# Kernel optimization log

Hardware: AMD Instinct MI355X
Metric: run time of the kernel (lower is better)

Reference implementation:

```python
import jax, jax.numpy as jnp
import numpy as np

T, S, F, A = 256, 256, 1024, 256


def setup_inputs() -> dict:
    key = jax.random.key(0)
    ks = jax.random.split(key, 7)
    scale = 0.02
    return {
        "batch_data": jax.random.normal(ks[0], (T * S, F), dtype=jnp.float32),
        "a_w": jax.random.normal(ks[1], (F, A), dtype=jnp.float32) * scale,
        "a_b": jax.random.normal(ks[2], (A,), dtype=jnp.float32) * scale,
        "b_w": jax.random.normal(ks[3], (F, A), dtype=jnp.float32) * scale,
        "b_b": jax.random.normal(ks[4], (A,), dtype=jnp.float32) * scale,
        "g_w": jax.random.normal(ks[5], (F, F), dtype=jnp.float32) * scale,
        "g_b": jax.random.normal(ks[6], (F,), dtype=jnp.float32) * scale,
        "s": S,
        "t": T,
    }


def reference(batch_data, a_w, a_b, b_w, b_b, g_w, g_b, s, t):
    # Linear projections then reshape to (t, s, dim)
    theta = (batch_data @ a_w + a_b).reshape(t, s, -1)   # (t, s, A)
    phi = (batch_data @ b_w + b_b).reshape(t, s, -1)     # (t, s, A)
    feats = (batch_data @ g_w + g_b).reshape(t, s, -1)   # (t, s, F)
    # Per-t bilinear attention: theta @ phi^T, no softmax
    attn = jnp.einsum("tsa,tra->tsr", theta, phi)        # (t, s, s)
    results = jnp.einsum("tsr,trf->tsf", attn, feats)    # (t, s, F)
    return results / (s + t)
```

## Files before the change

### kernel.cpp

```cpp
#include <hip/hip_runtime.h>
#include <stdint.h>

#define TT 256
#define SS 256
#define FF 1024
#define AA 256

typedef __attribute__((ext_vector_type(8))) short short8;
typedef __attribute__((ext_vector_type(4))) float floatx4;

__device__ __forceinline__ unsigned short f2bf(float f) {
  unsigned int u = __float_as_uint(f);
  u += 0x7FFFu + ((u >> 16) & 1u);
  return (unsigned short)(u >> 16);
}

__device__ __forceinline__ void gl_lds16(const unsigned short* g, unsigned short* l) {
  __builtin_amdgcn_global_load_lds(
      (__attribute__((address_space(1))) void*)(g),
      (__attribute__((address_space(3))) void*)(l), 16, 0, 0);
}

__global__ void k_transpose_cvt(const float* __restrict__ W,
                                unsigned short* __restrict__ WT,
                                int K, int N) {
  __shared__ float tile[32][33];
  const int bk = blockIdx.x * 32, bn = blockIdx.y * 32;
  const int tx = threadIdx.x, ty = threadIdx.y;
  for (int i = ty; i < 32; i += 8)
    tile[i][tx] = W[(size_t)(bk + i) * N + bn + tx];
  __syncthreads();
  for (int i = ty; i < 32; i += 8)
    WT[(size_t)(bn + i) * K + bk + tx] = f2bf(tile[tx][i]);
}

__global__ __launch_bounds__(256) void k_cvt(const float* __restrict__ in,
                                             unsigned short* __restrict__ out,
                                             unsigned int n8) {
  unsigned int i = blockIdx.x * 256u + threadIdx.x;
  const unsigned int stride = gridDim.x * 256u;
  for (; i < n8; i += stride) {
    const size_t base = (size_t)i * 8;
    const floatx4 v0 = *(const floatx4*)(in + base);
    const floatx4 v1 = *(const floatx4*)(in + base + 4);
    ushort4 h0, h1;
    h0.x = f2bf(v0.x); h0.y = f2bf(v0.y); h0.z = f2bf(v0.z); h0.w = f2bf(v0.w);
    h1.x = f2bf(v1.x); h1.y = f2bf(v1.y); h1.z = f2bf(v1.z); h1.w = f2bf(v1.w);
    *(ushort4*)(out + base) = h0;
    *(ushort4*)(out + base + 4) = h1;
  }
}

__device__ __forceinline__ void stage_half(const unsigned short* G, int ld,
                                           unsigned short* L, int tid) {
  const int wave = tid >> 6, lane = tid & 63;
#pragma unroll
  for (int c = 0; c < 2; ++c) {
    const int chunk = c * 8 + wave;
    const int r = chunk * 8 + (lane >> 3);
    const int k8 = (lane & 7) ^ (lane >> 3);
    gl_lds16(G + (size_t)r * ld + k8 * 8, L + chunk * 512);
  }
}

__device__ __forceinline__ short8 ldsfrag(const unsigned short* h, int row,
                                          int col) {
  return *(const short8*)&h[row * 64 + (col ^ ((row & 7) << 3))];
}

#define KLOOP_256(Ap, ldA, Bp, ldB, NKT)                                       \
  for (int kt = 0; kt < (NKT); ++kt) {                                         \
    const unsigned short* Ah = As + ((kt & 1) * 2 + wm) * 8192;                \
    const unsigned short* Bh = Bs + ((kt & 1) * 2 + (wn >> 1)) * 8192;         \
    const int nbuf = 1 - (kt & 1);                                             \
    if (kt + 1 < (NKT)) {                                                      \
      stage_half((Ap) + (size_t)(kt + 1) * 64, (ldA),                          \
                 As + (nbuf * 2 + 0) * 8192, tid);                             \
      asm volatile("s_waitcnt vmcnt(6)" ::: "memory");                         \
    } else {                                                                   \
      asm volatile("s_waitcnt vmcnt(0)" ::: "memory");                         \
    }                                                                          \
    asm volatile("s_barrier" ::: "memory");                                    \
    _Pragma("unroll") for (int i = 0; i < 4; ++i)                              \
        _Pragma("unroll") for (int ks = 0; ks < 2; ++ks)                       \
            af[i][ks] = ldsfrag(Ah, i * 16 + lr, ks * 32 + lq * 8);            \
    _Pragma("unroll") for (int j = 0; j < 4; ++j)                              \
        _Pragma("unroll") for (int ks = 0; ks < 2; ++ks)                       \
            bf[j][ks] = ldsfrag(Bh, brow + j * 16 + lr, ks * 32 + lq * 8);     \
    __builtin_amdgcn_s_setprio(1);                                             \
    _Pragma("unroll") for (int i = 0; i < 4; ++i)                              \
        _Pragma("unroll") for (int j = 0; j < 2; ++j)                          \
            _Pragma("unroll") for (int ks = 0; ks < 2; ++ks)                   \
                acc[i][j] = __builtin_amdgcn_mfma_f32_16x16x32_bf16(           \
                    af[i][ks], bf[j][ks], acc[i][j], 0, 0, 0);                 \
    __builtin_amdgcn_s_setprio(0);                                             \
    asm volatile("s_barrier" ::: "memory");                                    \
    if (kt + 1 < (NKT))                                                        \
      stage_half((Ap) + 128 * (ldA) + (size_t)(kt + 1) * 64, (ldA),            \
                 As + (nbuf * 2 + 1) * 8192, tid);                             \
    _Pragma("unroll") for (int i = 0; i < 4; ++i)                              \
        _Pragma("unroll") for (int ks = 0; ks < 2; ++ks)                       \
            af1[i][ks] = ldsfrag(Ah, 64 + i * 16 + lr, ks * 32 + lq * 8);      \
    __builtin_amdgcn_s_setprio(1);                                             \
    _Pragma("unroll") for (int i = 0; i < 4; ++i)                              \
        _Pragma("unroll") for (int j = 0; j < 2; ++j)                          \
            _Pragma("unroll") for (int ks = 0; ks < 2; ++ks)                   \
                acc[i][2 + j] = __builtin_amdgcn_mfma_f32_16x16x32_bf16(       \
                    af[i][ks], bf[2 + j][ks], acc[i][2 + j], 0, 0, 0);         \
    __builtin_amdgcn_s_setprio(0);                                             \
    asm volatile("s_barrier" ::: "memory");                                    \
    if (kt + 2 < (NKT))                                                        \
      stage_half((Bp) + (size_t)(kt + 2) * 64, (ldB),                          \
                 Bs + ((kt & 1) * 2 + 0) * 8192, tid);                         \
    __builtin_amdgcn_s_setprio(1);                                             \
    _Pragma("unroll") for (int i = 0; i < 4; ++i)                              \
        _Pragma("unroll") for (int j = 0; j < 2; ++j)                          \
            _Pragma("unroll") for (int ks = 0; ks < 2; ++ks)                   \
                acc[4 + i][j] = __builtin_amdgcn_mfma_f32_16x16x32_bf16(       \
                    af1[i][ks], bf[j][ks], acc[4 + i][j], 0, 0, 0);            \
    __builtin_amdgcn_s_setprio(0);                                             \
    asm volatile("s_barrier" ::: "memory");                                    \
    if (kt + 2 < (NKT))                                                        \
      stage_half((Bp) + 128 * (ldB) + (size_t)(kt + 2) * 64, (ldB),            \
                 Bs + ((kt & 1) * 2 + 1) * 8192, tid);                         \
    __builtin_amdgcn_s_setprio(1);                                             \
    _Pragma("unroll") for (int i = 0; i < 4; ++i)                              \
        _Pragma("unroll") for (int j = 0; j < 2; ++j)                          \
            _Pragma("unroll") for (int ks = 0; ks < 2; ++ks)                   \
                acc[4 + i][2 + j] = __builtin_amdgcn_mfma_f32_16x16x32_bf16(   \
                    af1[i][ks], bf[2 + j][ks], acc[4 + i][2 + j], 0, 0, 0);    \
    __builtin_amdgcn_s_setprio(0);                                             \
    asm volatile("s_barrier" ::: "memory");                                    \
  }

#define PROLOGUE_256(Ap, ldA, Bp, ldB)                                         \
  stage_half((Bp), (ldB), Bs + 0 * 8192, tid);                                 \
  stage_half((Bp) + 128 * (ldB), (ldB), Bs + 1 * 8192, tid);                   \
  stage_half((Ap), (ldA), As + 0 * 8192, tid);                                 \
  stage_half((Ap) + 128 * (ldA), (ldA), As + 1 * 8192, tid);                   \
  stage_half((Bp) + 64, (ldB), Bs + 2 * 8192, tid);                            \
  stage_half((Bp) + 128 * (ldB) + 64, (ldB), Bs + 3 * 8192, tid);

__global__ __launch_bounds__(512, 2) void k_proj3(
    const unsigned short* __restrict__ batchH,
    const unsigned short* __restrict__ aT,
    const unsigned short* __restrict__ bT,
    const unsigned short* __restrict__ gT,
    const float* __restrict__ a_b, const float* __restrict__ b_b,
    const float* __restrict__ g_b,
    unsigned short* __restrict__ theta,
    unsigned short* __restrict__ phi,
    unsigned short* __restrict__ featsT,
    int mbase) {
  __shared__ unsigned short lds[65536];
  unsigned short* As = lds;
  unsigned short* Bs = lds + 32768;

  const int nwg = gridDim.x;
  const int hb = blockIdx.x;
  const int logical = (hb & 7) * (nwg >> 3) + (hb >> 3);
  const int nt = logical % 6;
  const int mtile = logical / 6;
  const int m0l = mtile * 256;
  const int m0 = mbase + m0l;

  const unsigned short* Wt; const float* bias; int nb0, mode;
  if (nt == 0)      { Wt = aT; bias = a_b; nb0 = 0;              mode = 0; }
  else if (nt == 1) { Wt = bT; bias = b_b; nb0 = 0;              mode = 1; }
  else              { Wt = gT; bias = g_b; nb0 = (nt - 2) * 256; mode = 2; }

  const int tid = threadIdx.x;
  const int wave = tid >> 6, lane = tid & 63;
  const int wm = wave >> 2, wn = wave & 3;
  const int lr = lane & 15, lq = lane >> 4;
  const int brow = (wn & 1) * 64;

  const unsigned short* Ap = batchH + (size_t)m0l * FF;
  const unsigned short* Bp = Wt + (size_t)nb0 * FF;

  floatx4 acc[8][4];
#pragma unroll
  for (int i = 0; i < 8; i++)
#pragma unroll
    for (int j = 0; j < 4; j++) acc[i][j] = (floatx4)0.0f;

  short8 af[4][2], af1[4][2], bf[4][2];

  PROLOGUE_256(Ap, FF, Bp, FF)
#pragma unroll 1
  KLOOP_256(Ap, FF, Bp, FF, FF / 64)

#pragma unroll
  for (int fi = 0; fi < 8; ++fi) {
    const int srow = wm * 128 + fi * 16 + lq * 4;
#pragma unroll
    for (int j = 0; j < 4; ++j) {
      const int col = wn * 64 + j * 16 + lr;
      const float bv = bias[nb0 + col];
      if (mode == 2) {
        const int t = m0 >> 8;
        ushort4 h;
        h.x = f2bf(acc[fi][j][0] + bv);
        h.y = f2bf(acc[fi][j][1] + bv);
        h.z = f2bf(acc[fi][j][2] + bv);
        h.w = f2bf(acc[fi][j][3] + bv);
        *(ushort4*)&featsT[((size_t)t * FF + nb0 + col) * SS + srow] = h;
      } else {
        unsigned short* outp = (mode == 0) ? theta : phi;
#pragma unroll
        for (int rr = 0; rr < 4; ++rr)
          outp[(size_t)(m0 + srow + rr) * AA + col] = f2bf(acc[fi][j][rr] + bv);
      }
    }
  }
}

template <bool OUTF32>
__global__ __launch_bounds__(512, 2) void k_bt256(
    const unsigned short* __restrict__ A, const unsigned short* __restrict__ B,
    void* __restrict__ C, int ldA, int ldB, int K,
    long sA, long sB, long sC, int ntiles, float scale) {
  __shared__ unsigned short lds[65536];
  unsigned short* As = lds;
  unsigned short* Bs = lds + 32768;

  const int nwg = gridDim.x;
  const int hb = blockIdx.x;
  const int logical = (nwg & 7) ? hb : (hb & 7) * (nwg >> 3) + (hb >> 3);
  const int bz = logical / ntiles;
  const int n0 = (logical % ntiles) * 256;

  const int tid = threadIdx.x;
  const int wave = tid >> 6, lane = tid & 63;
  const int wm = wave >> 2, wn = wave & 3;
  const int lr = lane & 15, lq = lane >> 4;
  const int brow = (wn & 1) * 64;

  const unsigned short* Ap = A + (size_t)bz * sA;
  const unsigned short* Bp = B + (size_t)bz * sB + (size_t)n0 * ldB;

  floatx4 acc[8][4];
#pragma unroll
  for (int i = 0; i < 8; i++)
#pragma unroll
    for (int j = 0; j < 4; j++) acc[i][j] = (floatx4)0.0f;

  short8 af[4][2], af1[4][2], bf[4][2];
  const int NKT = K / 64;

  PROLOGUE_256(Ap, ldA, Bp, ldB)
#pragma unroll 1
  KLOOP_256(Ap, ldA, Bp, ldB, NKT)

  const int ldC = ntiles * 256;
#pragma unroll
  for (int fi = 0; fi < 8; ++fi) {
    const int srow = wm * 128 + fi * 16 + lq * 4;
#pragma unroll
    for (int j = 0; j < 4; ++j) {
      const int col = n0 + wn * 64 + j * 16 + lr;
#pragma unroll
      for (int rr = 0; rr < 4; ++rr) {
        const float v = acc[fi][j][rr] * scale;
        if (OUTF32) {
          float* Cb = (float*)C + (size_t)bz * sC;
          Cb[(size_t)(srow + rr) * ldC + col] = v;
        } else {
          unsigned short* Cb = (unsigned short*)C + (size_t)bz * sC;
          Cb[(size_t)(srow + rr) * ldC + col] = f2bf(v);
        }
      }
    }
  }
}

extern "C" void kernel_launch(void* const* d_in, const int* in_sizes, int n_in,
                              void* d_out, int out_size, void* d_ws,
                              size_t ws_size, hipStream_t stream) {
  const float* batch = (const float*)d_in[0];
  const float* a_w   = (const float*)d_in[1];
  const float* a_b   = (const float*)d_in[2];
  const float* b_w   = (const float*)d_in[3];
  const float* b_b   = (const float*)d_in[4];
  const float* g_w   = (const float*)d_in[5];
  const float* g_b   = (const float*)d_in[6];
  float* out = (float*)d_out;

  unsigned short* ws     = (unsigned short*)d_ws;
  unsigned short* aT     = ws;
  unsigned short* bT     = aT + (size_t)AA * FF;
  unsigned short* gT     = bT + (size_t)AA * FF;
  unsigned short* theta  = gT + (size_t)FF * FF;
  unsigned short* phi    = theta + (size_t)TT * SS * AA;
  unsigned short* featsT = phi + (size_t)TT * SS * AA;
  unsigned short* attn   = featsT + (size_t)TT * FF * SS;

  dim3 tb(32, 8);
  k_transpose_cvt<<<dim3(32, 8),  tb, 0, stream>>>(a_w, aT, FF, AA);
  k_transpose_cvt<<<dim3(32, 8),  tb, 0, stream>>>(b_w, bT, FF, AA);
  k_transpose_cvt<<<dim3(32, 32), tb, 0, stream>>>(g_w, gT, FF, FF);

  const size_t base_bytes  = 238026752ull;
  const size_t batch_bytes = (size_t)TT * SS * FF * 2;
  if (ws_size >= base_bytes + batch_bytes) {
    unsigned short* batchH = attn + (size_t)TT * SS * SS;
    k_cvt<<<2048, 256, 0, stream>>>(batch, batchH,
                                    (unsigned int)((size_t)TT * SS * FF / 8));
    k_proj3<<<6 * 256, 512, 0, stream>>>(batchH, aT, bT, gT, a_b, b_b, g_b,
                                         theta, phi, featsT, 0);
  } else {
    unsigned short* batchH = attn;
    const int CHUNK_ROWS = 16384;
    for (int c = 0; c < 4; c++) {
      const float* src = batch + (size_t)c * CHUNK_ROWS * FF;
      k_cvt<<<2048, 256, 0, stream>>>(
          src, batchH, (unsigned int)((size_t)CHUNK_ROWS * FF / 8));
      k_proj3<<<6 * 64, 512, 0, stream>>>(batchH, aT, bT, gT, a_b, b_b, g_b,
                                          theta, phi, featsT, c * CHUNK_ROWS);
    }
  }

  k_bt256<false><<<TT, 512, 0, stream>>>(
      theta, phi, attn, AA, AA, AA,
      (long)SS * AA, (long)SS * AA, (long)SS * SS, 1, 1.0f);

  k_bt256<true><<<4 * TT, 512, 0, stream>>>(
      attn, featsT, out, SS, SS, SS,
      (long)SS * SS, (long)FF * SS, (long)SS * FF, 4, 1.0f / 512.0f);
}
```

Before: 434.6 us.

## Fuse fp32-to-bf16 conversion of batch into projection GEMM A-tile loading

Removes the separate conversion kernel that wrote a bf16 copy of the 256MB fp32 batch. The projection GEMM now loads fp32 rows straight into registers, converts them to bf16, and writes them into the swizzled LDS tile, with a restructured software pipeline that interleaves these loads and writes with the MFMA phases. This saves a full extra write and reread of the batch. In exchange, each of the six N-tiles per M-tile rereads the fp32 batch, twice the bytes of the old bf16 reads, and it adds register pressure and VALU conversion work inside the main loop.

```diff
diff --git a/kernel.cpp b/kernel.cpp
--- a/kernel.cpp
+++ b/kernel.cpp
@@ -34,23 +34,6 @@
     WT[(size_t)(bn + i) * K + bk + tx] = f2bf(tile[tx][i]);
 }
 
-__global__ __launch_bounds__(256) void k_cvt(const float* __restrict__ in,
-                                             unsigned short* __restrict__ out,
-                                             unsigned int n8) {
-  unsigned int i = blockIdx.x * 256u + threadIdx.x;
-  const unsigned int stride = gridDim.x * 256u;
-  for (; i < n8; i += stride) {
-    const size_t base = (size_t)i * 8;
-    const floatx4 v0 = *(const floatx4*)(in + base);
-    const floatx4 v1 = *(const floatx4*)(in + base + 4);
-    ushort4 h0, h1;
-    h0.x = f2bf(v0.x); h0.y = f2bf(v0.y); h0.z = f2bf(v0.z); h0.w = f2bf(v0.w);
-    h1.x = f2bf(v1.x); h1.y = f2bf(v1.y); h1.z = f2bf(v1.z); h1.w = f2bf(v1.w);
-    *(ushort4*)(out + base) = h0;
-    *(ushort4*)(out + base + 4) = h1;
-  }
-}
-
 __device__ __forceinline__ void stage_half(const unsigned short* G, int ld,
                                            unsigned short* L, int tid) {
   const int wave = tid >> 6, lane = tid & 63;
@@ -66,6 +49,34 @@
 __device__ __forceinline__ short8 ldsfrag(const unsigned short* h, int row,
                                           int col) {
   return *(const short8*)&h[row * 64 + (col ^ ((row & 7) << 3))];
+}
+
+struct A4 { floatx4 v0, v1, v2, v3; };
+
+__device__ __forceinline__ A4 a_load(const float* G, int ar, int ag) {
+  const float* p = G + (size_t)ar * FF + ag * 8;
+  A4 a;
+  a.v0 = *(const floatx4*)(p);
+  a.v1 = *(const floatx4*)(p + 4);
+  a.v2 = *(const floatx4*)(p + 8);
+  a.v3 = *(const floatx4*)(p + 12);
+  return a;
+}
+
+__device__ __forceinline__ void a_write(unsigned short* L, int ar, int ag,
+                                        const A4& a) {
+  short8 h0, h1;
+  h0[0] = (short)f2bf(a.v0.x); h0[1] = (short)f2bf(a.v0.y);
+  h0[2] = (short)f2bf(a.v0.z); h0[3] = (short)f2bf(a.v0.w);
+  h0[4] = (short)f2bf(a.v1.x); h0[5] = (short)f2bf(a.v1.y);
+  h0[6] = (short)f2bf(a.v1.z); h0[7] = (short)f2bf(a.v1.w);
+  h1[0] = (short)f2bf(a.v2.x); h1[1] = (short)f2bf(a.v2.y);
+  h1[2] = (short)f2bf(a.v2.z); h1[3] = (short)f2bf(a.v2.w);
+  h1[4] = (short)f2bf(a.v3.x); h1[5] = (short)f2bf(a.v3.y);
+  h1[6] = (short)f2bf(a.v3.z); h1[7] = (short)f2bf(a.v3.w);
+  const int s = ar & 7;
+  *(short8*)&L[ar * 64 + ((ag ^ s) * 8)] = h0;
+  *(short8*)&L[ar * 64 + (((ag + 1) ^ s) * 8)] = h1;
 }
 
 #define KLOOP_256(Ap, ldA, Bp, ldB, NKT)                                       \
@@ -141,8 +152,8 @@
   stage_half((Bp) + 64, (ldB), Bs + 2 * 8192, tid);                            \
   stage_half((Bp) + 128 * (ldB) + 64, (ldB), Bs + 3 * 8192, tid);
 
-__global__ __launch_bounds__(512, 2) void k_proj3(
-    const unsigned short* __restrict__ batchH,
+__global__ __launch_bounds__(512, 2) void k_proj4(
+    const float* __restrict__ batchF,
     const unsigned short* __restrict__ aT,
     const unsigned short* __restrict__ bT,
     const unsigned short* __restrict__ gT,
@@ -150,8 +161,7 @@
     const float* __restrict__ g_b,
     unsigned short* __restrict__ theta,
     unsigned short* __restrict__ phi,
-    unsigned short* __restrict__ featsT,
-    int mbase) {
+    unsigned short* __restrict__ featsT) {
   __shared__ unsigned short lds[65536];
   unsigned short* As = lds;
   unsigned short* Bs = lds + 32768;
@@ -161,8 +171,7 @@
   const int logical = (hb & 7) * (nwg >> 3) + (hb >> 3);
   const int nt = logical % 6;
   const int mtile = logical / 6;
-  const int m0l = mtile * 256;
-  const int m0 = mbase + m0l;
+  const int m0 = mtile * 256;
 
   const unsigned short* Wt; const float* bias; int nb0, mode;
   if (nt == 0)      { Wt = aT; bias = a_b; nb0 = 0;              mode = 0; }
@@ -174,8 +183,10 @@
   const int wm = wave >> 2, wn = wave & 3;
   const int lr = lane & 15, lq = lane >> 4;
   const int brow = (wn & 1) * 64;
-
-  const unsigned short* Ap = batchH + (size_t)m0l * FF;
+  const int ar = tid >> 2;
+  const int ag = (tid & 3) * 2;
+
+  const float* Apf = batchF + (size_t)m0 * FF;
   const unsigned short* Bp = Wt + (size_t)nb0 * FF;
 
   floatx4 acc[8][4];
@@ -185,10 +196,107 @@
     for (int j = 0; j < 4; j++) acc[i][j] = (floatx4)0.0f;
 
   short8 af[4][2], af1[4][2], bf[4][2];
-
-  PROLOGUE_256(Ap, FF, Bp, FF)
+  A4 a0s, a1s;
+  const int NKT = FF / 64;
+
+  stage_half(Bp,                 FF, Bs + 0 * 8192, tid);
+  stage_half(Bp + 128 * FF,      FF, Bs + 1 * 8192, tid);
+  a0s = a_load(Apf,            ar, ag);
+  a1s = a_load(Apf + 128 * FF, ar, ag);
+  stage_half(Bp + 64,            FF, Bs + 2 * 8192, tid);
+  stage_half(Bp + 128 * FF + 64, FF, Bs + 3 * 8192, tid);
+  a_write(As + 0 * 8192, ar, ag, a0s);
+  a_write(As + 1 * 8192, ar, ag, a1s);
+  asm volatile("s_waitcnt lgkmcnt(0)" ::: "memory");
+  asm volatile("s_barrier" ::: "memory");
+
 #pragma unroll 1
-  KLOOP_256(Ap, FF, Bp, FF, FF / 64)
+  for (int kt = 0; kt < NKT; ++kt) {
+    const unsigned short* Ah = As + ((kt & 1) * 2 + wm) * 8192;
+    const unsigned short* Bh = Bs + ((kt & 1) * 2 + (wn >> 1)) * 8192;
+    const int nbuf = 1 - (kt & 1);
+
+    if (kt + 1 < NKT) {
+      a0s = a_load(Apf + (size_t)(kt + 1) * 64, ar, ag);
+      asm volatile("s_waitcnt vmcnt(8)" ::: "memory");
+    } else {
+      asm volatile("s_waitcnt vmcnt(0)" ::: "memory");
+    }
+    asm volatile("s_barrier" ::: "memory");
+#pragma unroll
+    for (int i = 0; i < 4; ++i)
+#pragma unroll
+      for (int ks = 0; ks < 2; ++ks)
+        af[i][ks] = ldsfrag(Ah, i * 16 + lr, ks * 32 + lq * 8);
+#pragma unroll
+    for (int j = 0; j < 4; ++j)
+#pragma unroll
+      for (int ks = 0; ks < 2; ++ks)
+        bf[j][ks] = ldsfrag(Bh, brow + j * 16 + lr, ks * 32 + lq * 8);
+    __builtin_amdgcn_s_setprio(1);
+#pragma unroll
+    for (int i = 0; i < 4; ++i)
+#pragma unroll
+      for (int j = 0; j < 2; ++j)
+#pragma unroll
+        for (int ks = 0; ks < 2; ++ks)
+          acc[i][j] = __builtin_amdgcn_mfma_f32_16x16x32_bf16(
+              af[i][ks], bf[j][ks], acc[i][j], 0, 0, 0);
+    __builtin_amdgcn_s_setprio(0);
+    asm volatile("s_barrier" ::: "memory");
+
+    if (kt + 1 < NKT)
+      a1s = a_load(Apf + 128 * FF + (size_t)(kt + 1) * 64, ar, ag);
+    __builtin_amdgcn_s_setprio(1);
+#pragma unroll
+    for (int i = 0; i < 4; ++i)
+#pragma unroll
+      for (int j = 0; j < 2; ++j)
+#pragma unroll
+        for (int ks = 0; ks < 2; ++ks)
+          acc[i][2 + j] = __builtin_amdgcn_mfma_f32_16x16x32_bf16(
+              af[i][ks], bf[2 + j][ks], acc[i][2 + j], 0, 0, 0);
+    __builtin_amdgcn_s_setprio(0);
+#pragma unroll
+    for (int i = 0; i < 4; ++i)
+#pragma unroll
+      for (int ks = 0; ks < 2; ++ks)
+        af1[i][ks] = ldsfrag(Ah, 64 + i * 16 + lr, ks * 32 + lq * 8);
+    asm volatile("s_barrier" ::: "memory");
+
+    if (kt + 1 < NKT) a_write(As + (nbuf * 2 + 0) * 8192, ar, ag, a0s);
+    if (kt + 2 < NKT)
+      stage_half(Bp + (size_t)(kt + 2) * 64, FF,
+                 Bs + ((kt & 1) * 2 + 0) * 8192, tid);
+    __builtin_amdgcn_s_setprio(1);
+#pragma unroll
+    for (int i = 0; i < 4; ++i)
+#pragma unroll
+      for (int j = 0; j < 2; ++j)
+#pragma unroll
+        for (int ks = 0; ks < 2; ++ks)
+          acc[4 + i][j] = __builtin_amdgcn_mfma_f32_16x16x32_bf16(
+              af1[i][ks], bf[j][ks], acc[4 + i][j], 0, 0, 0);
+    __builtin_amdgcn_s_setprio(0);
+    asm volatile("s_barrier" ::: "memory");
+
+    if (kt + 1 < NKT) a_write(As + (nbuf * 2 + 1) * 8192, ar, ag, a1s);
+    if (kt + 2 < NKT)
+      stage_half(Bp + 128 * FF + (size_t)(kt + 2) * 64, FF,
+                 Bs + ((kt & 1) * 2 + 1) * 8192, tid);
+    __builtin_amdgcn_s_setprio(1);
+#pragma unroll
+    for (int i = 0; i < 4; ++i)
+#pragma unroll
+      for (int j = 0; j < 2; ++j)
+#pragma unroll
+        for (int ks = 0; ks < 2; ++ks)
+          acc[4 + i][2 + j] = __builtin_amdgcn_mfma_f32_16x16x32_bf16(
+              af1[i][ks], bf[2 + j][ks], acc[4 + i][2 + j], 0, 0, 0);
+    __builtin_amdgcn_s_setprio(0);
+    asm volatile("s_waitcnt lgkmcnt(0)" ::: "memory");
+    asm volatile("s_barrier" ::: "memory");
+  }
 
 #pragma unroll
   for (int fi = 0; fi < 8; ++fi) {
@@ -300,25 +408,8 @@
   k_transpose_cvt<<<dim3(32, 8),  tb, 0, stream>>>(b_w, bT, FF, AA);
   k_transpose_cvt<<<dim3(32, 32), tb, 0, stream>>>(g_w, gT, FF, FF);
 
-  const size_t base_bytes  = 238026752ull;
-  const size_t batch_bytes = (size_t)TT * SS * FF * 2;
-  if (ws_size >= base_bytes + batch_bytes) {
-    unsigned short* batchH = attn + (size_t)TT * SS * SS;
-    k_cvt<<<2048, 256, 0, stream>>>(batch, batchH,
-                                    (unsigned int)((size_t)TT * SS * FF / 8));
-    k_proj3<<<6 * 256, 512, 0, stream>>>(batchH, aT, bT, gT, a_b, b_b, g_b,
-                                         theta, phi, featsT, 0);
-  } else {
-    unsigned short* batchH = attn;
-    const int CHUNK_ROWS = 16384;
-    for (int c = 0; c < 4; c++) {
-      const float* src = batch + (size_t)c * CHUNK_ROWS * FF;
-      k_cvt<<<2048, 256, 0, stream>>>(
-          src, batchH, (unsigned int)((size_t)CHUNK_ROWS * FF / 8));
-      k_proj3<<<6 * 64, 512, 0, stream>>>(batchH, aT, bT, gT, a_b, b_b, g_b,
-                                          theta, phi, featsT, c * CHUNK_ROWS);
-    }
-  }
+  k_proj4<<<6 * 256, 512, 0, stream>>>(batch, aT, bT, gT, a_b, b_b, g_b,
+                                       theta, phi, featsT);
 
   k_bt256<false><<<TT, 512, 0, stream>>>(
       theta, phi, attn, AA, AA, AA,
```

Measured after the change: 465.4 us. 1.07x slower.
